# Kernel optimization log

Measured on AMD Instinct MI355X. Metric: run time of the kernel, lower is better.

Reference implementation:

```python
import jax, jax.numpy as jnp
import numpy as np

N_NODES = 100000
N_EDGES = 800000
F_IN = 128
H1, C1 = 8, 32
N_CLS = 40
NEG_SLOPE = 0.2


def setup_inputs() -> dict:
    key = jax.random.key(0)
    ks = jax.random.split(key, 10)
    s = 1.0 / np.sqrt(F_IN)
    s2 = 1.0 / np.sqrt(H1 * C1)
    return {
        "x": jax.random.normal(ks[0], (N_NODES, F_IN), jnp.float32),
        "edge_index": jax.random.randint(ks[1], (2, N_EDGES), 0, N_NODES, jnp.int64),
        "W1": jax.random.normal(ks[2], (F_IN, H1 * C1), jnp.float32) * s,
        "a_src1": jax.random.normal(ks[3], (H1, C1), jnp.float32) * s2,
        "a_dst1": jax.random.normal(ks[4], (H1, C1), jnp.float32) * s2,
        "b1": jnp.zeros((H1 * C1,), jnp.float32),
        "W2": jax.random.normal(ks[5], (H1 * C1, N_CLS), jnp.float32) * s2,
        "a_src2": jax.random.normal(ks[6], (1, N_CLS), jnp.float32) * 0.1,
        "a_dst2": jax.random.normal(ks[7], (1, N_CLS), jnp.float32) * 0.1,
        "b2": jnp.zeros((N_CLS,), jnp.float32),
    }


def gat_conv(x, src, dst, W, a_src, a_dst, b, heads, out_ch, concat):
    n = x.shape[0]
    h = (x @ W).reshape(n, heads, out_ch)            # [N,H,C]
    alpha_s = jnp.einsum("nhc,hc->nh", h, a_src)     # [N,H]
    alpha_d = jnp.einsum("nhc,hc->nh", h, a_dst)
    e = alpha_s[src] + alpha_d[dst]                  # [E,H]
    e = jax.nn.leaky_relu(e, NEG_SLOPE)
    # per-destination segment softmax (stable)
    m = jax.ops.segment_max(e, dst, num_segments=n)  # [N,H]
    e = jnp.exp(e - m[dst])
    denom = jax.ops.segment_sum(e, dst, num_segments=n)
    alpha = e / (denom[dst] + 1e-16)                 # [E,H]
    msg = alpha[:, :, None] * h[src]                 # [E,H,C]
    out = jax.ops.segment_sum(msg, dst, num_segments=n)  # [N,H,C]
    out = out.reshape(n, heads * out_ch) if concat else out.mean(axis=1)
    return out + b


def reference(x, edge_index, W1, a_src1, a_dst1, b1, W2, a_src2, a_dst2, b2):
    n = x.shape[0]
    # PyG GATConv default add_self_loops=True
    loop = jnp.arange(n, dtype=edge_index.dtype)
    src = jnp.concatenate([edge_index[0], loop])
    dst = jnp.concatenate([edge_index[1], loop])
    # dropout layers are identity in eval mode
    h = gat_conv(x, src, dst, W1, a_src1, a_dst1, b1, H1, C1, concat=True)
    h = jax.nn.elu(h)
    out = gat_conv(h, src, dst, W2, a_src2, a_dst2, b2, 1, N_CLS, concat=False)
    return jax.nn.log_softmax(out, axis=1)
```

## Files before the change

### kernel.cpp

```cpp
#include <hip/hip_runtime.h>
#include <hip/hip_fp16.h>
#include <math.h>

#define N_NODESc 100000
#define N_EDGESc 800000
#define F_INc    128
#define HC1c     256
#define NCLSc    40
#define NEG_SLOPEc 0.2f
#define CAPc     40
#define CSH      4

typedef _Float16 half8 __attribute__((ext_vector_type(8)));
typedef __fp16   f16x2 __attribute__((ext_vector_type(2)));
typedef float    f32x4 __attribute__((ext_vector_type(4)));
typedef float    f32x2 __attribute__((ext_vector_type(2)));

__device__ __forceinline__ unsigned pack_ws(float w, int src) {
    union { f16x2 h; unsigned u; } t;
    t.h = __builtin_amdgcn_cvt_pkrtz(w, w);
    return (unsigned)src | ((t.u & 0xFFFFu) << 17);
}
__device__ __forceinline__ float unpack_w(unsigned pe) {
    union { unsigned short s; __fp16 h; } t;
    t.s = (unsigned short)(pe >> 17);
    return (float)t.h;
}


__global__ void k_init(const float* __restrict__ W1, const float* __restrict__ W2,
                       _Float16* __restrict__ W1Tf, _Float16* __restrict__ W2Tf,
                       int* __restrict__ cnt) {
    if (blockIdx.x < 22) {
        int f = blockIdx.x * 256 + threadIdx.x;
        if (f < 4096) {
            int lane16 = f & 15, quad = (f >> 4) & 3, k0 = (f >> 6) & 3, jt = f >> 8;
            int c = lane16 * 16 + jt;
            int kbase = k0 * 32 + quad * 8;
            _Float16* o = W1Tf + (size_t)f * 8;
            #pragma unroll
            for (int j = 0; j < 8; j++) o[j] = (_Float16)W1[(kbase + j) * HC1c + c];
        } else if (f < 4096 + 1536) {
            int g = f - 4096;
            int lane16 = g & 15, quad = (g >> 4) & 3, k0 = (g >> 6) & 7, jt = g >> 9;
            int c = jt * 16 + lane16;
            int kbase = k0 * 32 + quad * 8;
            _Float16* o = W2Tf + (size_t)g * 8;
            #pragma unroll
            for (int j = 0; j < 8; j++)
                o[j] = (c < NCLSc) ? (_Float16)W2[(kbase + j) * NCLSc + c] : (_Float16)0.f;
        }
    } else {
        int i = (blockIdx.x - 22) * 256 + threadIdx.x;
        if (i < N_NODESc * 4) ((int4*)cnt)[i] = (int4){0, 0, 0, 0};
    }
}


__global__ __launch_bounds__(256) void k_gemm1_scatter(
    const float* __restrict__ x, const _Float16* __restrict__ W1Tf,
    const float* __restrict__ a_src1, const float* __restrict__ a_dst1,
    unsigned char* __restrict__ h1f8, float* __restrict__ as1, float* __restrict__ ad1,
    const int* __restrict__ src, const int* __restrict__ dst,
    int* __restrict__ cnt, int* __restrict__ bucket) {
    if ((blockIdx.x & 1) == 0) {
        int i = (blockIdx.x >> 1) * 256 + threadIdx.x;
        if (i < N_EDGESc / 4) {
            int4 s = ((const int4*)src)[i];
            int4 d = ((const int4*)dst)[i];
            int p0 = atomicAdd(&cnt[d.x << CSH], 1);
            int p1 = atomicAdd(&cnt[d.y << CSH], 1);
            int p2 = atomicAdd(&cnt[d.z << CSH], 1);
            int p3 = atomicAdd(&cnt[d.w << CSH], 1);
            if (p0 < CAPc) __builtin_nontemporal_store(s.x, &bucket[d.x * CAPc + p0]);
            if (p1 < CAPc) __builtin_nontemporal_store(s.y, &bucket[d.y * CAPc + p1]);
            if (p2 < CAPc) __builtin_nontemporal_store(s.z, &bucket[d.z * CAPc + p2]);
            if (p3 < CAPc) __builtin_nontemporal_store(s.w, &bucket[d.w * CAPc + p3]);
        }
        return;
    }
    int wave = ((blockIdx.x >> 1) * 256 + (int)threadIdx.x) >> 6;
    int n0 = wave * 16;
    if (n0 >= N_NODESc) return;
    int L = threadIdx.x & 63, lane16 = L & 15, quad = L >> 4;
    f32x4 acc[16];
    #pragma unroll
    for (int jt = 0; jt < 16; jt++) acc[jt] = (f32x4){0.f, 0.f, 0.f, 0.f};
    const float* A = x + (size_t)(n0 + lane16) * F_INc + quad * 8;
    const _Float16* Bf = W1Tf + L * 8;
    #pragma unroll
    for (int k0 = 0; k0 < 4; k0++) {
        float4 f0 = *(const float4*)(A + k0 * 32);
        float4 f1 = *(const float4*)(A + k0 * 32 + 4);
        union { half8 v; f16x2 h[4]; } af;
        af.h[0] = __builtin_amdgcn_cvt_pkrtz(f0.x, f0.y);
        af.h[1] = __builtin_amdgcn_cvt_pkrtz(f0.z, f0.w);
        af.h[2] = __builtin_amdgcn_cvt_pkrtz(f1.x, f1.y);
        af.h[3] = __builtin_amdgcn_cvt_pkrtz(f1.z, f1.w);
        #pragma unroll
        for (int jt = 0; jt < 16; jt++) {
            half8 bf = *(const half8*)(Bf + (jt * 4 + k0) * 512);
            acc[jt] = __builtin_amdgcn_mfma_f32_16x16x32_f16(af.v, bf, acc[jt], 0, 0, 0);
        }
    }
    {
        #pragma unroll
        for (int r = 0; r < 4; r++) {
            uint4 st;
            int d;
            d = __builtin_amdgcn_cvt_pk_fp8_f32(acc[0][r], acc[1][r], 0, false);
            d = __builtin_amdgcn_cvt_pk_fp8_f32(acc[2][r], acc[3][r], d, true);
            st.x = (unsigned)d;
            d = __builtin_amdgcn_cvt_pk_fp8_f32(acc[4][r], acc[5][r], 0, false);
            d = __builtin_amdgcn_cvt_pk_fp8_f32(acc[6][r], acc[7][r], d, true);
            st.y = (unsigned)d;
            d = __builtin_amdgcn_cvt_pk_fp8_f32(acc[8][r], acc[9][r], 0, false);
            d = __builtin_amdgcn_cvt_pk_fp8_f32(acc[10][r], acc[11][r], d, true);
            st.z = (unsigned)d;
            d = __builtin_amdgcn_cvt_pk_fp8_f32(acc[12][r], acc[13][r], 0, false);
            d = __builtin_amdgcn_cvt_pk_fp8_f32(acc[14][r], acc[15][r], d, true);
            st.w = (unsigned)d;
            *(uint4*)(h1f8 + (size_t)(n0 + quad * 4 + r) * HC1c + lane16 * 16) = st;
        }
    }
    {
        float asv[16], adv[16];
        const float4* ap = (const float4*)(a_src1 + lane16 * 16);
        const float4* dp = (const float4*)(a_dst1 + lane16 * 16);
        #pragma unroll
        for (int q = 0; q < 4; q++) {
            float4 a4 = ap[q], d4 = dp[q];
            asv[4*q] = a4.x; asv[4*q+1] = a4.y; asv[4*q+2] = a4.z; asv[4*q+3] = a4.w;
            adv[4*q] = d4.x; adv[4*q+1] = d4.y; adv[4*q+2] = d4.z; adv[4*q+3] = d4.w;
        }
        float ps[4] = {0,0,0,0}, pd[4] = {0,0,0,0};
        #pragma unroll
        for (int jt = 0; jt < 16; jt++) {
            #pragma unroll
            for (int r = 0; r < 4; r++) {
                ps[r] += acc[jt][r] * asv[jt];
                pd[r] += acc[jt][r] * adv[jt];
            }
        }
        #pragma unroll
        for (int r = 0; r < 4; r++) {
            ps[r] += __shfl_xor(ps[r], 1);
            pd[r] += __shfl_xor(pd[r], 1);
        }
        if ((lane16 & 1) == 0) {
            int h = lane16 >> 1;
            #pragma unroll
            for (int r = 0; r < 4; r++) {
                int n = n0 + quad * 4 + r;
                as1[n * 8 + h] = ps[r];
                ad1[n * 8 + h] = pd[r];
            }
        }
    }
}


__global__ __launch_bounds__(256) void k_agg1(
    const int* __restrict__ cnt, const int* __restrict__ bucket,
    const float* __restrict__ as1, const float* __restrict__ ad1,
    const unsigned char* __restrict__ h1f8, const float* __restrict__ b1,
    _Float16* __restrict__ act1b) {
    int n = blockIdx.x * 4 + (threadIdx.x >> 6);
    if (n >= N_NODESc) return;
    int L = threadIdx.x & 63;
    int eL = L >> 3, hL = L & 7;
    int hA = L >> 3;
    int beg = n * CAPc;
    int end = beg + min(cnt[n << CSH], CAPc);
    float ad = ad1[n * 8 + hL];
    float vs = as1[n * 8 + hL] + ad;
    float s_self = (vs > 0.f) ? vs : NEG_SLOPEc * vs;
    float m_run = s_self, d_run = 1.f;
    unsigned ldself = *((const unsigned*)(h1f8 + (size_t)n * HC1c) + L);
    f32x2 accA = __builtin_amdgcn_cvt_pk_f32_fp8((int)ldself, false);
    f32x2 accB = __builtin_amdgcn_cvt_pk_f32_fp8((int)ldself, true);
    for (int base = beg; base < end; base += 16) {
        int m = min(16, end - base);
        int src0 = 0, src1 = 0;
        float s0 = -INFINITY, s1 = -INFINITY;
        if (eL < m) {
            src0 = bucket[base + eL];
            float v = as1[src0 * 8 + hL] + ad;
            s0 = (v > 0.f) ? v : NEG_SLOPEc * v;
        }
        if (eL + 8 < m) {
            src1 = bucket[base + eL + 8];
            float v = as1[src1 * 8 + hL] + ad;
            s1 = (v > 0.f) ? v : NEG_SLOPEc * v;
        }
        float mc = fmaxf(s0, s1);
        mc = fmaxf(mc, __shfl_xor(mc, 8));
        mc = fmaxf(mc, __shfl_xor(mc, 16));
        mc = fmaxf(mc, __shfl_xor(mc, 32));
        float mnew = fmaxf(m_run, mc);
        float w0 = (eL < m) ? __expf(s0 - mnew) : 0.f;
        float w1 = (eL + 8 < m) ? __expf(s1 - mnew) : 0.f;
        float wsum = w0 + w1;
        wsum += __shfl_xor(wsum, 8);
        wsum += __shfl_xor(wsum, 16);
        wsum += __shfl_xor(wsum, 32);
        float scale = __expf(m_run - mnew);
        d_run = d_run * scale + wsum;
        m_run = mnew;
        float sc = __shfl(scale, hA);
        f32x2 sc2 = (f32x2){sc, sc};
        accA *= sc2;
        accB *= sc2;
        unsigned pk0 = pack_ws(w0, src0);
        unsigned pk1 = pack_ws(w1, src1);
        #pragma unroll
        for (int r = 0; r < 4; r++) {
            int e0 = r * 4;
            if (e0 < m) {
                unsigned pk = (e0 < 8) ? pk0 : pk1;
                unsigned pe[4]; unsigned ld[4];
                #pragma unroll
                for (int j = 0; j < 4; j++)
                    pe[j] = __shfl(pk, ((e0 + j) & 7) * 8 + hA);
                #pragma unroll
                for (int j = 0; j < 4; j++)
                    ld[j] = *((const unsigned*)(h1f8 + (size_t)(pe[j] & 0x1FFFFu) * HC1c) + L);
                #pragma unroll
                for (int j = 0; j < 4; j++) {
                    float w = unpack_w(pe[j]);
                    f32x2 wv = (f32x2){w, w};
                    f32x2 lo = __builtin_amdgcn_cvt_pk_f32_fp8((int)ld[j], false);
                    f32x2 hi = __builtin_amdgcn_cvt_pk_f32_fp8((int)ld[j], true);
                    asm("v_pk_fma_f32 %0, %1, %2, %0" : "+v"(accA) : "v"(wv), "v"(lo));
                    asm("v_pk_fma_f32 %0, %1, %2, %0" : "+v"(accB) : "v"(wv), "v"(hi));
                }
            }
        }
    }
    float inv = __builtin_amdgcn_rcpf(d_run + 1e-16f);
    float inv_h = __shfl(inv, hA);
    float4 bb = ((const float4*)b1)[L];
    float o0 = accA[0] * inv_h + bb.x;
    float o1 = accA[1] * inv_h + bb.y;
    float o2 = accB[0] * inv_h + bb.z;
    float o3 = accB[1] * inv_h + bb.w;
    o0 = (o0 > 0.f) ? o0 : (__expf(o0) - 1.f);
    o1 = (o1 > 0.f) ? o1 : (__expf(o1) - 1.f);
    o2 = (o2 > 0.f) ? o2 : (__expf(o2) - 1.f);
    o3 = (o3 > 0.f) ? o3 : (__expf(o3) - 1.f);
    union { uint2 u; f16x2 h[2]; } st;
    st.h[0] = __builtin_amdgcn_cvt_pkrtz(o0, o1);
    st.h[1] = __builtin_amdgcn_cvt_pkrtz(o2, o3);
    ((uint2*)(act1b + (size_t)n * HC1c))[L] = st.u;
}


__global__ __launch_bounds__(256) void k_gemm2(
    const _Float16* __restrict__ act1b, const _Float16* __restrict__ W2Tf,
    const float* __restrict__ a_src2, const float* __restrict__ a_dst2,
    _Float16* __restrict__ h2b, float* __restrict__ as2, float* __restrict__ ad2) {
    int wave = (blockIdx.x * 256 + threadIdx.x) >> 6;
    int n0 = wave * 16;
    if (n0 >= N_NODESc) return;
    int L = threadIdx.x & 63, lane16 = L & 15, quad = L >> 4;
    f32x4 acc[3];
    #pragma unroll
    for (int jt = 0; jt < 3; jt++) acc[jt] = (f32x4){0.f, 0.f, 0.f, 0.f};
    const _Float16* A = act1b + (size_t)(n0 + lane16) * HC1c + quad * 8;
    const _Float16* Bf = W2Tf + L * 8;
    #pragma unroll
    for (int k0 = 0; k0 < 8; k0++) {
        half8 af = *(const half8*)(A + k0 * 32);
        #pragma unroll
        for (int jt = 0; jt < 3; jt++) {
            half8 bf = *(const half8*)(Bf + (jt * 8 + k0) * 512);
            acc[jt] = __builtin_amdgcn_mfma_f32_16x16x32_f16(af, bf, acc[jt], 0, 0, 0);
        }
    }
    float ps[4] = {0.f, 0.f, 0.f, 0.f}, pd[4] = {0.f, 0.f, 0.f, 0.f};
    #pragma unroll
    for (int jt = 0; jt < 3; jt++) {
        int col = jt * 16 + lane16;
        float ws = (col < NCLSc) ? a_src2[col] : 0.f;
        float wd = (col < NCLSc) ? a_dst2[col] : 0.f;
        #pragma unroll
        for (int r = 0; r < 4; r++) {
            float v = acc[jt][r];
            int n = n0 + quad * 4 + r;
            if (col < NCLSc) h2b[(size_t)n * NCLSc + col] = (_Float16)v;
            ps[r] += v * ws; pd[r] += v * wd;
        }
    }
    #pragma unroll
    for (int r = 0; r < 4; r++) {
        float s = ps[r], d = pd[r];
        s += __shfl_xor(s, 1); d += __shfl_xor(d, 1);
        s += __shfl_xor(s, 2); d += __shfl_xor(d, 2);
        s += __shfl_xor(s, 4); d += __shfl_xor(d, 4);
        s += __shfl_xor(s, 8); d += __shfl_xor(d, 8);
        if (lane16 == 0) {
            int n = n0 + quad * 4 + r;
            as2[n] = s; ad2[n] = d;
        }
    }
}


__global__ __launch_bounds__(256) void k_agg2(
    const int* __restrict__ cnt, const int* __restrict__ bucket,
    const float* __restrict__ as2, const float* __restrict__ ad2,
    const _Float16* __restrict__ h2b, const float* __restrict__ b2,
    float* __restrict__ out) {
    int L = threadIdx.x & 63;
    int half = L >> 5, l32 = L & 31;
    int n = blockIdx.x * 8 + (int)(threadIdx.x >> 6) * 2 + half;
    int beg = n * CAPc;
    int end = beg + min(cnt[n << CSH], CAPc);
    float ad = ad2[n];
    float vs = as2[n] + ad;
    float s_self = (vs > 0.f) ? vs : NEG_SLOPEc * vs;
    float m_run = s_self, d_run = 1.f;
    f16x2 acc2 = (f16x2){(__fp16)0.f, (__fp16)0.f};
    if (l32 < 20) {
        union { unsigned u; f16x2 h; } pk;
        pk.u = *((const unsigned*)(h2b + (size_t)n * NCLSc) + l32);
        acc2 = pk.h;
    }
    for (int base = beg; base < end; base += 32) {
        int m = min(32, end - base);
        int src = 0; float s = -INFINITY;
        if (l32 < m) {
            src = bucket[base + l32];
            float v = as2[src] + ad;
            s = (v > 0.f) ? v : NEG_SLOPEc * v;
        }
        float mc = s;
        #pragma unroll
        for (int o = 16; o; o >>= 1) mc = fmaxf(mc, __shfl_xor(mc, o));
        float mnew = fmaxf(m_run, mc);
        float w = (l32 < m) ? __expf(s - mnew) : 0.f;
        float ws = w;
        #pragma unroll
        for (int o = 16; o; o >>= 1) ws += __shfl_xor(ws, o);
        float scale = __expf(m_run - mnew);
        d_run = d_run * scale + ws;
        m_run = mnew;
        f16x2 sc2 = __builtin_amdgcn_cvt_pkrtz(scale, scale);
        acc2 *= sc2;
        for (int jb = 0; jb < m; jb += 3) {
            float wv[3]; int sev[3]; unsigned ldv[3];
            #pragma unroll
            for (int r = 0; r < 3; r++) {
                int e = jb + r;
                int lane = half * 32 + (e & 31);
                wv[r] = __shfl(w, lane);
                sev[r] = __shfl(src, lane);
                if (e >= m) wv[r] = 0.f;
            }
            #pragma unroll
            for (int r = 0; r < 3; r++) {
                ldv[r] = 0u;
                if (l32 < 20)
                    ldv[r] = *((const unsigned*)(h2b + (size_t)sev[r] * NCLSc) + l32);
            }
            #pragma unroll
            for (int r = 0; r < 3; r++) {
                f16x2 we2 = __builtin_amdgcn_cvt_pkrtz(wv[r], wv[r]);
                union { unsigned u; f16x2 h; } pk; pk.u = ldv[r];
                acc2 += we2 * pk.h;
            }
        }
    }
    float vx = -INFINITY, vy = -INFINITY;
    if (l32 < 20) {
        float2 bb = ((const float2*)b2)[l32];
        float inv = __builtin_amdgcn_rcpf(d_run + 1e-16f);
        vx = (float)acc2[0] * inv + bb.x;
        vy = (float)acc2[1] * inv + bb.y;
    }
    float mv = fmaxf(vx, vy);
    #pragma unroll
    for (int o = 16; o; o >>= 1) mv = fmaxf(mv, __shfl_xor(mv, o));
    float ex = (l32 < 20) ? __expf(vx - mv) + __expf(vy - mv) : 0.f;
    #pragma unroll
    for (int o = 16; o; o >>= 1) ex += __shfl_xor(ex, o);
    float ls = __logf(ex);
    if (l32 < 20) {
        float2 o2; o2.x = vx - mv - ls; o2.y = vy - mv - ls;
        ((float2*)(out + (size_t)n * NCLSc))[l32] = o2;
    }
}


extern "C" void kernel_launch(void* const* d_in, const int* in_sizes, int n_in,
                              void* d_out, int out_size, void* d_ws, size_t ws_size,
                              hipStream_t stream) {
    const float* x    = (const float*)d_in[0];
    const int*   ei   = (const int*)d_in[1];
    const float* W1   = (const float*)d_in[2];
    const float* as1w = (const float*)d_in[3];
    const float* ad1w = (const float*)d_in[4];
    const float* b1   = (const float*)d_in[5];
    const float* W2   = (const float*)d_in[6];
    const float* as2w = (const float*)d_in[7];
    const float* ad2w = (const float*)d_in[8];
    const float* b2   = (const float*)d_in[9];
    float* out = (float*)d_out;

    char* p = (char*)d_ws;
    unsigned char* h1f8 = (unsigned char*)p; p += (size_t)N_NODESc * HC1c;
    _Float16* act1b = (_Float16*)p; p += (size_t)N_NODESc * HC1c * 2;
    _Float16* W1Tf  = (_Float16*)p; p += (size_t)4096 * 8 * 2;
    _Float16* W2Tf  = (_Float16*)p; p += (size_t)1536 * 8 * 2;
    float* a_s1 = (float*)p; p += (size_t)N_NODESc * 8 * 4;
    float* a_d1 = (float*)p; p += (size_t)N_NODESc * 8 * 4;
    _Float16* h2b = (_Float16*)p; p += (size_t)N_NODESc * NCLSc * 2;
    float* a_s2 = (float*)p; p += (size_t)N_NODESc * 4;
    float* a_d2 = (float*)p; p += (size_t)N_NODESc * 4;
    int* cnt    = (int*)p;   p += (size_t)N_NODESc * 16 * 4;
    int* bucket = (int*)p;   p += (size_t)N_NODESc * CAPc * 4;
    (void)ws_size; (void)in_sizes; (void)n_in; (void)out_size;

    const int* src = ei;
    const int* dst = ei + N_EDGESc;

    k_init<<<22 + (N_NODESc * 4 + 255) / 256, 256, 0, stream>>>(W1, W2, W1Tf, W2Tf, cnt);

    int nwave_blk = ((N_NODESc + 15) / 16 + 3) / 4;
    k_gemm1_scatter<<<nwave_blk * 2, 256, 0, stream>>>(
        x, W1Tf, as1w, ad1w, h1f8, a_s1, a_d1, src, dst, cnt, bucket);

    k_agg1<<<(N_NODESc + 3) / 4, 256, 0, stream>>>(cnt, bucket, a_s1, a_d1, h1f8, b1, act1b);
    k_gemm2<<<nwave_blk, 256, 0, stream>>>(act1b, W2Tf, as2w, ad2w, h2b, a_s2, a_d2);
    k_agg2<<<N_NODESc / 8, 256, 0, stream>>>(cnt, bucket, a_s2, a_d2, h2b, b2, out);
}
```

Baseline: 280.1 us.

## Fuse layer-1 aggregation with layer-2 GEMM through LDS; compact edge counters

The layer-1 aggregation and the layer-2 projection GEMM become one kernel. Each block aggregates 16 nodes (four per wave), writes the ELU'd fp16 activations into swizzled shared memory, then three waves run the MFMA for the 40 output columns and reduce the attention logits through LDS. This removes the global round trip of the 100000x256 fp16 activation buffer and one kernel launch. Separately, the per-node counters are no longer padded to 16 ints each, which shrinks the init memset but puts many counters on the same cache lines, so atomics in the scatter may contend. Each block now serialises four node aggregations per wave and leaves one wave idle during the GEMM, which lowers parallelism.

After: 278.6 us. Within noise of the previous version (-0.5%).

```diff
diff --git a/kernel.cpp b/kernel.cpp
--- a/kernel.cpp
+++ b/kernel.cpp
@@ -9,7 +9,6 @@
 #define NCLSc    40
 #define NEG_SLOPEc 0.2f
 #define CAPc     40
-#define CSH      4
 
 typedef _Float16 half8 __attribute__((ext_vector_type(8)));
 typedef __fp16   f16x2 __attribute__((ext_vector_type(2)));
@@ -52,7 +51,7 @@
         }
     } else {
         int i = (blockIdx.x - 22) * 256 + threadIdx.x;
-        if (i < N_NODESc * 4) ((int4*)cnt)[i] = (int4){0, 0, 0, 0};
+        if (i < N_NODESc / 4) ((int4*)cnt)[i] = (int4){0, 0, 0, 0};
     }
 }
 
@@ -68,10 +67,10 @@
         if (i < N_EDGESc / 4) {
             int4 s = ((const int4*)src)[i];
             int4 d = ((const int4*)dst)[i];
-            int p0 = atomicAdd(&cnt[d.x << CSH], 1);
-            int p1 = atomicAdd(&cnt[d.y << CSH], 1);
-            int p2 = atomicAdd(&cnt[d.z << CSH], 1);
-            int p3 = atomicAdd(&cnt[d.w << CSH], 1);
+            int p0 = atomicAdd(&cnt[d.x], 1);
+            int p1 = atomicAdd(&cnt[d.y], 1);
+            int p2 = atomicAdd(&cnt[d.z], 1);
+            int p3 = atomicAdd(&cnt[d.w], 1);
             if (p0 < CAPc) __builtin_nontemporal_store(s.x, &bucket[d.x * CAPc + p0]);
             if (p1 < CAPc) __builtin_nontemporal_store(s.y, &bucket[d.y * CAPc + p1]);
             if (p2 < CAPc) __builtin_nontemporal_store(s.z, &bucket[d.z * CAPc + p2]);
@@ -160,148 +159,152 @@
 }
 
 
-__global__ __launch_bounds__(256) void k_agg1(
+__global__ __launch_bounds__(256) void k_agg1_g2(
     const int* __restrict__ cnt, const int* __restrict__ bucket,
     const float* __restrict__ as1, const float* __restrict__ ad1,
     const unsigned char* __restrict__ h1f8, const float* __restrict__ b1,
-    _Float16* __restrict__ act1b) {
-    int n = blockIdx.x * 4 + (threadIdx.x >> 6);
-    if (n >= N_NODESc) return;
+    const _Float16* __restrict__ W2Tf, const float* __restrict__ a_src2,
+    const float* __restrict__ a_dst2, _Float16* __restrict__ h2b,
+    float* __restrict__ as2, float* __restrict__ ad2) {
+    __shared__ _Float16 sact[16 * HC1c];
+    __shared__ float sp[3][16], sd[3][16];
     int L = threadIdx.x & 63;
+    int wid = threadIdx.x >> 6;
     int eL = L >> 3, hL = L & 7;
     int hA = L >> 3;
-    int beg = n * CAPc;
-    int end = beg + min(cnt[n << CSH], CAPc);
-    float ad = ad1[n * 8 + hL];
-    float vs = as1[n * 8 + hL] + ad;
-    float s_self = (vs > 0.f) ? vs : NEG_SLOPEc * vs;
-    float m_run = s_self, d_run = 1.f;
-    unsigned ldself = *((const unsigned*)(h1f8 + (size_t)n * HC1c) + L);
-    f32x2 accA = __builtin_amdgcn_cvt_pk_f32_fp8((int)ldself, false);
-    f32x2 accB = __builtin_amdgcn_cvt_pk_f32_fp8((int)ldself, true);
-    for (int base = beg; base < end; base += 16) {
-        int m = min(16, end - base);
-        int src0 = 0, src1 = 0;
-        float s0 = -INFINITY, s1 = -INFINITY;
-        if (eL < m) {
-            src0 = bucket[base + eL];
-            float v = as1[src0 * 8 + hL] + ad;
-            s0 = (v > 0.f) ? v : NEG_SLOPEc * v;
-        }
-        if (eL + 8 < m) {
-            src1 = bucket[base + eL + 8];
-            float v = as1[src1 * 8 + hL] + ad;
-            s1 = (v > 0.f) ? v : NEG_SLOPEc * v;
-        }
-        float mc = fmaxf(s0, s1);
-        mc = fmaxf(mc, __shfl_xor(mc, 8));
-        mc = fmaxf(mc, __shfl_xor(mc, 16));
-        mc = fmaxf(mc, __shfl_xor(mc, 32));
-        float mnew = fmaxf(m_run, mc);
-        float w0 = (eL < m) ? __expf(s0 - mnew) : 0.f;
-        float w1 = (eL + 8 < m) ? __expf(s1 - mnew) : 0.f;
-        float wsum = w0 + w1;
-        wsum += __shfl_xor(wsum, 8);
-        wsum += __shfl_xor(wsum, 16);
-        wsum += __shfl_xor(wsum, 32);
-        float scale = __expf(m_run - mnew);
-        d_run = d_run * scale + wsum;
-        m_run = mnew;
-        float sc = __shfl(scale, hA);
-        f32x2 sc2 = (f32x2){sc, sc};
-        accA *= sc2;
-        accB *= sc2;
-        unsigned pk0 = pack_ws(w0, src0);
-        unsigned pk1 = pack_ws(w1, src1);
-        #pragma unroll
-        for (int r = 0; r < 4; r++) {
-            int e0 = r * 4;
-            if (e0 < m) {
-                unsigned pk = (e0 < 8) ? pk0 : pk1;
-                unsigned pe[4]; unsigned ld[4];
-                #pragma unroll
-                for (int j = 0; j < 4; j++)
-                    pe[j] = __shfl(pk, ((e0 + j) & 7) * 8 + hA);
-                #pragma unroll
-                for (int j = 0; j < 4; j++)
-                    ld[j] = *((const unsigned*)(h1f8 + (size_t)(pe[j] & 0x1FFFFu) * HC1c) + L);
-                #pragma unroll
-                for (int j = 0; j < 4; j++) {
-                    float w = unpack_w(pe[j]);
-                    f32x2 wv = (f32x2){w, w};
-                    f32x2 lo = __builtin_amdgcn_cvt_pk_f32_fp8((int)ld[j], false);
-                    f32x2 hi = __builtin_amdgcn_cvt_pk_f32_fp8((int)ld[j], true);
-                    asm("v_pk_fma_f32 %0, %1, %2, %0" : "+v"(accA) : "v"(wv), "v"(lo));
-                    asm("v_pk_fma_f32 %0, %1, %2, %0" : "+v"(accB) : "v"(wv), "v"(hi));
+    float4 bb = ((const float4*)b1)[L];
+    #pragma unroll 1
+    for (int nn = 0; nn < 4; nn++) {
+        int row = wid * 4 + nn;
+        int n = blockIdx.x * 16 + row;
+        int beg = n * CAPc;
+        int end = beg + min(cnt[n], CAPc);
+        float ad = ad1[n * 8 + hL];
+        float vs = as1[n * 8 + hL] + ad;
+        float s_self = (vs > 0.f) ? vs : NEG_SLOPEc * vs;
+        float m_run = s_self, d_run = 1.f;
+        unsigned ldself = *((const unsigned*)(h1f8 + (size_t)n * HC1c) + L);
+        f32x2 accA = __builtin_amdgcn_cvt_pk_f32_fp8((int)ldself, false);
+        f32x2 accB = __builtin_amdgcn_cvt_pk_f32_fp8((int)ldself, true);
+        for (int base = beg; base < end; base += 16) {
+            int m = min(16, end - base);
+            int src0 = 0, src1 = 0;
+            float s0 = -INFINITY, s1 = -INFINITY;
+            if (eL < m) {
+                src0 = bucket[base + eL];
+                float v = as1[src0 * 8 + hL] + ad;
+                s0 = (v > 0.f) ? v : NEG_SLOPEc * v;
+            }
+            if (eL + 8 < m) {
+                src1 = bucket[base + eL + 8];
+                float v = as1[src1 * 8 + hL] + ad;
+                s1 = (v > 0.f) ? v : NEG_SLOPEc * v;
+            }
+            float mc = fmaxf(s0, s1);
+            mc = fmaxf(mc, __shfl_xor(mc, 8));
+            mc = fmaxf(mc, __shfl_xor(mc, 16));
+            mc = fmaxf(mc, __shfl_xor(mc, 32));
+            float mnew = fmaxf(m_run, mc);
+            float w0 = (eL < m) ? __expf(s0 - mnew) : 0.f;
+            float w1 = (eL + 8 < m) ? __expf(s1 - mnew) : 0.f;
+            float wsum = w0 + w1;
+            wsum += __shfl_xor(wsum, 8);
+            wsum += __shfl_xor(wsum, 16);
+            wsum += __shfl_xor(wsum, 32);
+            float scale = __expf(m_run - mnew);
+            d_run = d_run * scale + wsum;
+            m_run = mnew;
+            float sc = __shfl(scale, hA);
+            f32x2 sc2 = (f32x2){sc, sc};
+            accA *= sc2;
+            accB *= sc2;
+            unsigned pk0 = pack_ws(w0, src0);
+            unsigned pk1 = pack_ws(w1, src1);
+            #pragma unroll
+            for (int r = 0; r < 4; r++) {
+                int e0 = r * 4;
+                if (e0 < m) {
+                    unsigned pk = (e0 < 8) ? pk0 : pk1;
+                    unsigned pe[4]; unsigned ld[4];
+                    #pragma unroll
+                    for (int j = 0; j < 4; j++)
+                        pe[j] = __shfl(pk, ((e0 + j) & 7) * 8 + hA);
+                    #pragma unroll
+                    for (int j = 0; j < 4; j++)
+                        ld[j] = *((const unsigned*)(h1f8 + (size_t)(pe[j] & 0x1FFFFu) * HC1c) + L);
+                    #pragma unroll
+                    for (int j = 0; j < 4; j++) {
+                        float w = unpack_w(pe[j]);
+                        f32x2 wv = (f32x2){w, w};
+                        f32x2 lo = __builtin_amdgcn_cvt_pk_f32_fp8((int)ld[j], false);
+                        f32x2 hi = __builtin_amdgcn_cvt_pk_f32_fp8((int)ld[j], true);
+                        asm("v_pk_fma_f32 %0, %1, %2, %0" : "+v"(accA) : "v"(wv), "v"(lo));
+                        asm("v_pk_fma_f32 %0, %1, %2, %0" : "+v"(accB) : "v"(wv), "v"(hi));
+                    }
                 }
             }
         }
-    }
-    float inv = __builtin_amdgcn_rcpf(d_run + 1e-16f);
-    float inv_h = __shfl(inv, hA);
-    float4 bb = ((const float4*)b1)[L];
-    float o0 = accA[0] * inv_h + bb.x;
-    float o1 = accA[1] * inv_h + bb.y;
-    float o2 = accB[0] * inv_h + bb.z;
-    float o3 = accB[1] * inv_h + bb.w;
-    o0 = (o0 > 0.f) ? o0 : (__expf(o0) - 1.f);
-    o1 = (o1 > 0.f) ? o1 : (__expf(o1) - 1.f);
-    o2 = (o2 > 0.f) ? o2 : (__expf(o2) - 1.f);
-    o3 = (o3 > 0.f) ? o3 : (__expf(o3) - 1.f);
-    union { uint2 u; f16x2 h[2]; } st;
-    st.h[0] = __builtin_amdgcn_cvt_pkrtz(o0, o1);
-    st.h[1] = __builtin_amdgcn_cvt_pkrtz(o2, o3);
-    ((uint2*)(act1b + (size_t)n * HC1c))[L] = st.u;
-}
-
-
-__global__ __launch_bounds__(256) void k_gemm2(
-    const _Float16* __restrict__ act1b, const _Float16* __restrict__ W2Tf,
-    const float* __restrict__ a_src2, const float* __restrict__ a_dst2,
-    _Float16* __restrict__ h2b, float* __restrict__ as2, float* __restrict__ ad2) {
-    int wave = (blockIdx.x * 256 + threadIdx.x) >> 6;
-    int n0 = wave * 16;
-    if (n0 >= N_NODESc) return;
-    int L = threadIdx.x & 63, lane16 = L & 15, quad = L >> 4;
-    f32x4 acc[3];
-    #pragma unroll
-    for (int jt = 0; jt < 3; jt++) acc[jt] = (f32x4){0.f, 0.f, 0.f, 0.f};
-    const _Float16* A = act1b + (size_t)(n0 + lane16) * HC1c + quad * 8;
-    const _Float16* Bf = W2Tf + L * 8;
-    #pragma unroll
-    for (int k0 = 0; k0 < 8; k0++) {
-        half8 af = *(const half8*)(A + k0 * 32);
-        #pragma unroll
-        for (int jt = 0; jt < 3; jt++) {
+        float inv = __builtin_amdgcn_rcpf(d_run + 1e-16f);
+        float inv_h = __shfl(inv, hA);
+        float o0 = accA[0] * inv_h + bb.x;
+        float o1 = accA[1] * inv_h + bb.y;
+        float o2 = accB[0] * inv_h + bb.z;
+        float o3 = accB[1] * inv_h + bb.w;
+        o0 = (o0 > 0.f) ? o0 : (__expf(o0) - 1.f);
+        o1 = (o1 > 0.f) ? o1 : (__expf(o1) - 1.f);
+        o2 = (o2 > 0.f) ? o2 : (__expf(o2) - 1.f);
+        o3 = (o3 > 0.f) ? o3 : (__expf(o3) - 1.f);
+        union { uint2 u; f16x2 h[2]; } st;
+        st.h[0] = __builtin_amdgcn_cvt_pkrtz(o0, o1);
+        st.h[1] = __builtin_amdgcn_cvt_pkrtz(o2, o3);
+        unsigned bofs = ((unsigned)(row * 512 + L * 8)) ^ ((unsigned)(row & 7) << 4);
+        *(uint2*)((char*)sact + bofs) = st.u;
+    }
+    __syncthreads();
+    if (wid < 3) {
+        int jt = wid;
+        int lane16 = L & 15, quad = L >> 4;
+        int n0 = blockIdx.x * 16;
+        f32x4 acc = (f32x4){0.f, 0.f, 0.f, 0.f};
+        const _Float16* Bf = W2Tf + L * 8;
+        unsigned rmask = ((unsigned)(lane16 & 7) << 4);
+        #pragma unroll
+        for (int k0 = 0; k0 < 8; k0++) {
+            unsigned abofs = ((unsigned)(lane16 * 512 + quad * 16 + k0 * 64)) ^ rmask;
+            half8 af = *(const half8*)((const char*)sact + abofs);
             half8 bf = *(const half8*)(Bf + (jt * 8 + k0) * 512);
-            acc[jt] = __builtin_amdgcn_mfma_f32_16x16x32_f16(af, bf, acc[jt], 0, 0, 0);
-        }
-    }
-    float ps[4] = {0.f, 0.f, 0.f, 0.f}, pd[4] = {0.f, 0.f, 0.f, 0.f};
-    #pragma unroll
-    for (int jt = 0; jt < 3; jt++) {
+            acc = __builtin_amdgcn_mfma_f32_16x16x32_f16(af, bf, acc, 0, 0, 0);
+        }
         int col = jt * 16 + lane16;
         float ws = (col < NCLSc) ? a_src2[col] : 0.f;
         float wd = (col < NCLSc) ? a_dst2[col] : 0.f;
+        float ps[4], pd[4];
         #pragma unroll
         for (int r = 0; r < 4; r++) {
-            float v = acc[jt][r];
+            float v = acc[r];
             int n = n0 + quad * 4 + r;
             if (col < NCLSc) h2b[(size_t)n * NCLSc + col] = (_Float16)v;
-            ps[r] += v * ws; pd[r] += v * wd;
-        }
-    }
-    #pragma unroll
-    for (int r = 0; r < 4; r++) {
-        float s = ps[r], d = pd[r];
-        s += __shfl_xor(s, 1); d += __shfl_xor(d, 1);
-        s += __shfl_xor(s, 2); d += __shfl_xor(d, 2);
-        s += __shfl_xor(s, 4); d += __shfl_xor(d, 4);
-        s += __shfl_xor(s, 8); d += __shfl_xor(d, 8);
-        if (lane16 == 0) {
-            int n = n0 + quad * 4 + r;
-            as2[n] = s; ad2[n] = d;
-        }
+            ps[r] = v * ws; pd[r] = v * wd;
+        }
+        #pragma unroll
+        for (int r = 0; r < 4; r++) {
+            float s = ps[r], d = pd[r];
+            s += __shfl_xor(s, 1); d += __shfl_xor(d, 1);
+            s += __shfl_xor(s, 2); d += __shfl_xor(d, 2);
+            s += __shfl_xor(s, 4); d += __shfl_xor(d, 4);
+            s += __shfl_xor(s, 8); d += __shfl_xor(d, 8);
+            if (lane16 == 0) {
+                sp[jt][quad * 4 + r] = s;
+                sd[jt][quad * 4 + r] = d;
+            }
+        }
+    }
+    __syncthreads();
+    if (threadIdx.x < 16) {
+        int r = threadIdx.x;
+        int n = blockIdx.x * 16 + r;
+        as2[n] = sp[0][r] + sp[1][r] + sp[2][r];
+        ad2[n] = sd[0][r] + sd[1][r] + sd[2][r];
     }
 }
 
@@ -315,7 +318,7 @@
     int half = L >> 5, l32 = L & 31;
     int n = blockIdx.x * 8 + (int)(threadIdx.x >> 6) * 2 + half;
     int beg = n * CAPc;
-    int end = beg + min(cnt[n << CSH], CAPc);
+    int end = beg + min(cnt[n], CAPc);
     float ad = ad2[n];
     float vs = as2[n] + ad;
     float s_self = (vs > 0.f) ? vs : NEG_SLOPEc * vs;
@@ -409,7 +412,6 @@
 
     char* p = (char*)d_ws;
     unsigned char* h1f8 = (unsigned char*)p; p += (size_t)N_NODESc * HC1c;
-    _Float16* act1b = (_Float16*)p; p += (size_t)N_NODESc * HC1c * 2;
     _Float16* W1Tf  = (_Float16*)p; p += (size_t)4096 * 8 * 2;
     _Float16* W2Tf  = (_Float16*)p; p += (size_t)1536 * 8 * 2;
     float* a_s1 = (float*)p; p += (size_t)N_NODESc * 8 * 4;
@@ -417,20 +419,21 @@
     _Float16* h2b = (_Float16*)p; p += (size_t)N_NODESc * NCLSc * 2;
     float* a_s2 = (float*)p; p += (size_t)N_NODESc * 4;
     float* a_d2 = (float*)p; p += (size_t)N_NODESc * 4;
-    int* cnt    = (int*)p;   p += (size_t)N_NODESc * 16 * 4;
+    int* cnt    = (int*)p;   p += (size_t)N_NODESc * 4;
     int* bucket = (int*)p;   p += (size_t)N_NODESc * CAPc * 4;
     (void)ws_size; (void)in_sizes; (void)n_in; (void)out_size;
 
     const int* src = ei;
     const int* dst = ei + N_EDGESc;
 
-    k_init<<<22 + (N_NODESc * 4 + 255) / 256, 256, 0, stream>>>(W1, W2, W1Tf, W2Tf, cnt);
+    k_init<<<22 + (N_NODESc / 4 + 255) / 256, 256, 0, stream>>>(W1, W2, W1Tf, W2Tf, cnt);
 
     int nwave_blk = ((N_NODESc + 15) / 16 + 3) / 4;
     k_gemm1_scatter<<<nwave_blk * 2, 256, 0, stream>>>(
         x, W1Tf, as1w, ad1w, h1f8, a_s1, a_d1, src, dst, cnt, bucket);
 
-    k_agg1<<<(N_NODESc + 3) / 4, 256, 0, stream>>>(cnt, bucket, a_s1, a_d1, h1f8, b1, act1b);
-    k_gemm2<<<nwave_blk, 256, 0, stream>>>(act1b, W2Tf, as2w, ad2w, h2b, a_s2, a_d2);
+    k_agg1_g2<<<N_NODESc / 16, 256, 0, stream>>>(
+        cnt, bucket, a_s1, a_d1, h1f8, b1, W2Tf, as2w, ad2w, h2b, a_s2, a_d2);
+
     k_agg2<<<N_NODESc / 8, 256, 0, stream>>>(cnt, bucket, a_s2, a_d2, h2b, b2, out);
 }
```
